# Performance work log

Measured on AMD Instinct MI355X. Metric: run time of the kernel, lower is better.

## Reference

```python
import jax, jax.numpy as jnp
import numpy as np

H = 256
OUT = 2
FANOUT = 10
RES_N = [200000, 50000, 12000, 4096]
USER_N = [250000, 60000, 20000, 8192]
B = RES_N[-1]


def setup_inputs() -> dict:
    key = jax.random.key(0)
    ks = jax.random.split(key, 40)
    ki = iter(ks)
    rng = np.random.default_rng(0)
    inp = {}
    inp["res_x"] = jax.random.normal(next(ki), (RES_N[0], H), jnp.float32)
    inp["user_x"] = jax.random.normal(next(ki), (USER_N[0], H), jnp.float32)
    for name, N in (("res", RES_N), ("user", USER_N)):
        for i in range(3):
            n_src, n_dst = N[i], N[i + 1]
            E = n_dst * FANOUT
            row = jax.random.randint(next(ki), (E,), 0, n_src)   # source node ids
            col = jnp.repeat(jnp.arange(n_dst), FANOUT)          # target node ids
            inp[f"{name}_ei{i}"] = jnp.stack([row, col]).astype(jnp.int32)
    counts = rng.integers(10, 31, size=B)                        # ragged users per restaurant
    T = int(counts.sum())
    inp["num_users_per_res"] = jnp.asarray(counts, jnp.int32)
    inp["inverse_idx"] = jax.random.randint(next(ki), (T,), 0, USER_N[-1])

    def lin(k, fi, fo):
        return jax.random.normal(k, (fo, fi), jnp.float32) / np.sqrt(fi)

    for name in ("res", "user"):
        for i in range(3):
            inp[f"{name}_Wl{i}"] = lin(next(ki), H, H)
            inp[f"{name}_bl{i}"] = jnp.zeros((H,), jnp.float32)
            inp[f"{name}_Wr{i}"] = lin(next(ki), H, H)
    inp["W_out"] = lin(next(ki), 2 * H, OUT)
    inp["b_out"] = jnp.zeros((OUT,), jnp.float32)
    return inp


def sage_conv(x_src, x_tgt, edge_index, Wl, bl, Wr):
    """PyG SAGEConv (aggr='mean', bipartite): lin_l(mean_j x_j) + lin_r(x_tgt)."""
    n_tgt = x_tgt.shape[0]
    msgs = x_src[edge_index[0]]                                            # [E, H] gather
    s = jax.ops.segment_sum(msgs, edge_index[1], num_segments=n_tgt)      # [n_tgt, H]
    cnt = jax.ops.segment_sum(jnp.ones((edge_index.shape[1],), x_src.dtype),
                              edge_index[1], num_segments=n_tgt)
    agg = s / jnp.maximum(cnt, 1.0)[:, None]
    return agg @ Wl.T + bl + x_tgt @ Wr.T


def gnn_forward(x, eis, params, N):
    # ReLU (and dropout, identity in eval) applied when i != num_layers-1 == 1
    for i, (ei, (Wl, bl, Wr)) in enumerate(zip(eis, params)):
        x_tgt = x[: N[i + 1]]
        x = sage_conv(x, x_tgt, ei, Wl, bl, Wr)
        if i != 1:
            x = jax.nn.relu(x)
    return x


def reference(res_x, user_x,
              res_ei0, res_ei1, res_ei2,
              user_ei0, user_ei1, user_ei2,
              inverse_idx, num_users_per_res,
              res_Wl0, res_bl0, res_Wr0,
              res_Wl1, res_bl1, res_Wr1,
              res_Wl2, res_bl2, res_Wr2,
              user_Wl0, user_bl0, user_Wr0,
              user_Wl1, user_bl1, user_Wr1,
              user_Wl2, user_bl2, user_Wr2,
              W_out, b_out):
    res_params = [(res_Wl0, res_bl0, res_Wr0), (res_Wl1, res_bl1, res_Wr1), (res_Wl2, res_bl2, res_Wr2)]
    user_params = [(user_Wl0, user_bl0, user_Wr0), (user_Wl1, user_bl1, user_Wr1), (user_Wl2, user_bl2, user_Wr2)]
    res_out = gnn_forward(res_x, (res_ei0, res_ei1, res_ei2), res_params, RES_N)      # [B, H]
    user_out = gnn_forward(user_x, (user_ei0, user_ei1, user_ei2), user_params, USER_N)  # [M, H]
    # ragged segment-mean pooling: split by num_users_per_res, mean each group
    u = user_out[inverse_idx]                                              # [T, H]
    T = inverse_idx.shape[0]
    seg_ids = jnp.repeat(jnp.arange(B), num_users_per_res, total_repeat_length=T)
    pooled = jax.ops.segment_sum(u, seg_ids, num_segments=B)
    pooled = pooled / num_users_per_res.astype(pooled.dtype)[:, None]      # [B, H]
    emb = jnp.concatenate([res_out, pooled], axis=1)                       # [B, 2H]
    return emb @ W_out.T + b_out
```

## Files before the change

kernel.cpp:

```cpp
#include <hip/hip_runtime.h>

#define H 256
#define FANOUT 10

typedef __attribute__((ext_vector_type(8))) short bf16x8;
typedef __attribute__((ext_vector_type(4))) float f32x4;

__device__ __forceinline__ unsigned short f2bf(float x) {
  unsigned int u = __float_as_uint(x);
  u += 0x7FFFu + ((u >> 16) & 1u);
  return (unsigned short)(u >> 16);
}
__device__ __forceinline__ float bf2f(unsigned short h) {
  return __uint_as_float(((unsigned int)h) << 16);
}

struct PtrPack { const float* p[12]; };

__global__ __launch_bounds__(256) void wprep_kernel(PtrPack pk,
                                                    unsigned short* __restrict__ WB) {
  int g = blockIdx.x * 256 + threadIdx.x;
  int mat = g >> 16;
  int e = g & 65535;
  float x = pk.p[mat][e];
  unsigned short h = f2bf(x);
  float r = x - bf2f(h);
  WB[(size_t)mat * 131072 + e] = h;
  WB[(size_t)mat * 131072 + 65536 + e] = f2bf(r);
}

__global__ __launch_bounds__(64) void agg_f32(
    const float* __restrict__ src, const int* __restrict__ row,
    unsigned short* __restrict__ ahi, unsigned short* __restrict__ alo, int n_tgt) {
  int t = blockIdx.x;
  if (t >= n_tgt) return;
  int tid = threadIdx.x;
  const int base = t * FANOUT;
  float4 acc = {0.f, 0.f, 0.f, 0.f};
#pragma unroll
  for (int k = 0; k < FANOUT; ++k) {
    int r = row[base + k];
    const float4 v = *reinterpret_cast<const float4*>(src + (size_t)r * H + tid * 4);
    acc.x += v.x; acc.y += v.y; acc.z += v.z; acc.w += v.w;
  }
  acc.x *= 0.1f; acc.y *= 0.1f; acc.z *= 0.1f; acc.w *= 0.1f;
  ushort4 h, l;
  h.x = f2bf(acc.x); l.x = f2bf(acc.x - bf2f(h.x));
  h.y = f2bf(acc.y); l.y = f2bf(acc.y - bf2f(h.y));
  h.z = f2bf(acc.z); l.z = f2bf(acc.z - bf2f(h.z));
  h.w = f2bf(acc.w); l.w = f2bf(acc.w - bf2f(h.w));
  *reinterpret_cast<ushort4*>(ahi + (size_t)t * H + tid * 4) = h;
  *reinterpret_cast<ushort4*>(alo + (size_t)t * H + tid * 4) = l;
}

__global__ __launch_bounds__(64) void agg_bf(
    const unsigned short* __restrict__ shi, const unsigned short* __restrict__ slo,
    const int* __restrict__ row,
    unsigned short* __restrict__ ahi, unsigned short* __restrict__ alo, int n_tgt) {
  int t = blockIdx.x;
  if (t >= n_tgt) return;
  int tid = threadIdx.x;
  const int base = t * FANOUT;
  float4 acc = {0.f, 0.f, 0.f, 0.f};
#pragma unroll
  for (int k = 0; k < FANOUT; ++k) {
    int r = row[base + k];
    size_t p = (size_t)r * H + tid * 4;
    const ushort4 vh = *reinterpret_cast<const ushort4*>(shi + p);
    const ushort4 vl = *reinterpret_cast<const ushort4*>(slo + p);
    acc.x += bf2f(vh.x) + bf2f(vl.x);
    acc.y += bf2f(vh.y) + bf2f(vl.y);
    acc.z += bf2f(vh.z) + bf2f(vl.z);
    acc.w += bf2f(vh.w) + bf2f(vl.w);
  }
  acc.x *= 0.1f; acc.y *= 0.1f; acc.z *= 0.1f; acc.w *= 0.1f;
  ushort4 h, l;
  h.x = f2bf(acc.x); l.x = f2bf(acc.x - bf2f(h.x));
  h.y = f2bf(acc.y); l.y = f2bf(acc.y - bf2f(h.y));
  h.z = f2bf(acc.z); l.z = f2bf(acc.z - bf2f(h.z));
  h.w = f2bf(acc.w); l.w = f2bf(acc.w - bf2f(h.w));
  *reinterpret_cast<ushort4*>(ahi + (size_t)t * H + tid * 4) = h;
  *reinterpret_cast<ushort4*>(alo + (size_t)t * H + tid * 4) = l;
}

template <int XT32>
__global__ __launch_bounds__(512, 1) void sage_gemm_mfma(
    const unsigned short* __restrict__ Ahi, const unsigned short* __restrict__ Alo,
    const unsigned short* __restrict__ Xhi, const unsigned short* __restrict__ Xlo,
    const float* __restrict__ Xf,
    const unsigned short* __restrict__ Wl2, const unsigned short* __restrict__ Wr2,
    const float* __restrict__ bias,
    unsigned short* __restrict__ Ohi, unsigned short* __restrict__ Olo,
    int n_tgt, int relu) {
  __shared__ unsigned short lds[2][2][128 * 32];
  const int tid = threadIdx.x;
  const int lane = tid & 63, wid = tid >> 6;
  const int wr = wid >> 2, wc = wid & 3;
  const int l15 = lane & 15, lk = lane >> 4;
  const int m0 = blockIdx.x * 128;
  const int srow = tid >> 2, sch = tid & 3;
  const int grow = m0 + srow;
  const bool sok = grow < n_tgt;

  f32x4 acc[4][4];
#pragma unroll
  for (int i = 0; i < 4; ++i)
#pragma unroll
    for (int j = 0; j < 4; ++j) acc[i][j] = (f32x4){0.f, 0.f, 0.f, 0.f};

  auto stage = [&](int buf, int s) {
    const int pass = s >> 3;
    const int kt = (s & 7) * 32;
    const int goff = grow * H + kt + sch * 8;
    bf16x8 vh = {0, 0, 0, 0, 0, 0, 0, 0};
    bf16x8 vl = {0, 0, 0, 0, 0, 0, 0, 0};
    if (sok) {
      if (pass == 0) {
        vh = *reinterpret_cast<const bf16x8*>(Ahi + goff);
        vl = *reinterpret_cast<const bf16x8*>(Alo + goff);
      } else if (XT32) {
        const float4 f0 = *reinterpret_cast<const float4*>(Xf + goff);
        const float4 f1 = *reinterpret_cast<const float4*>(Xf + goff + 4);
        const float xs[8] = {f0.x, f0.y, f0.z, f0.w, f1.x, f1.y, f1.z, f1.w};
#pragma unroll
        for (int i = 0; i < 8; ++i) {
          unsigned short h = f2bf(xs[i]);
          vh[i] = (short)h;
          vl[i] = (short)f2bf(xs[i] - bf2f(h));
        }
      } else {
        vh = *reinterpret_cast<const bf16x8*>(Xhi + goff);
        vl = *reinterpret_cast<const bf16x8*>(Xlo + goff);
      }
    }
    *reinterpret_cast<bf16x8*>(&lds[buf][0][srow * 32 + sch * 8]) = vh;
    *reinterpret_cast<bf16x8*>(&lds[buf][1][srow * 32 + sch * 8]) = vl;
  };

  stage(0, 0);
  __syncthreads();

  for (int s = 0; s < 16; ++s) {
    const int buf = s & 1;
    if (s < 15) stage(buf ^ 1, s + 1);
    const int pass = s >> 3;
    const int kt = (s & 7) * 32;
    const unsigned short* __restrict__ W = pass ? Wr2 : Wl2;
    bf16x8 bh[4], bl[4];
#pragma unroll
    for (int nf = 0; nf < 4; ++nf) {
      const int n = wc * 64 + nf * 16 + l15;
      const int off = n * H + kt + lk * 8;
      bh[nf] = *reinterpret_cast<const bf16x8*>(W + off);
      bl[nf] = *reinterpret_cast<const bf16x8*>(W + 65536 + off);
    }
    bf16x8 ah[4], al[4];
#pragma unroll
    for (int mf = 0; mf < 4; ++mf) {
      const int soff = (wr * 64 + mf * 16 + l15) * 32 + lk * 8;
      ah[mf] = *reinterpret_cast<const bf16x8*>(&lds[buf][0][soff]);
      al[mf] = *reinterpret_cast<const bf16x8*>(&lds[buf][1][soff]);
    }
#pragma unroll
    for (int mf = 0; mf < 4; ++mf)
#pragma unroll
      for (int nf = 0; nf < 4; ++nf) {
        acc[mf][nf] = __builtin_amdgcn_mfma_f32_16x16x32_bf16(ah[mf], bh[nf], acc[mf][nf], 0, 0, 0);
        acc[mf][nf] = __builtin_amdgcn_mfma_f32_16x16x32_bf16(ah[mf], bl[nf], acc[mf][nf], 0, 0, 0);
        acc[mf][nf] = __builtin_amdgcn_mfma_f32_16x16x32_bf16(al[mf], bh[nf], acc[mf][nf], 0, 0, 0);
      }
    __syncthreads();
  }

#pragma unroll
  for (int nf = 0; nf < 4; ++nf) {
    const int c = wc * 64 + nf * 16 + l15;
    const float bv = bias[c];
#pragma unroll
    for (int mf = 0; mf < 4; ++mf) {
      const int r0 = m0 + wr * 64 + mf * 16 + lk * 4;
#pragma unroll
      for (int j = 0; j < 4; ++j) {
        const int r = r0 + j;
        if (r < n_tgt) {
          float v = acc[mf][nf][j] + bv;
          if (relu) v = fmaxf(v, 0.f);
          unsigned short h = f2bf(v);
          Ohi[(size_t)r * H + c] = h;
          Olo[(size_t)r * H + c] = f2bf(v - bf2f(h));
        }
      }
    }
  }
}

__global__ __launch_bounds__(1024) void scan_kernel(
    const int* __restrict__ cnt, int* __restrict__ off, int B) {
  __shared__ int sdata[1024];
  const int t = threadIdx.x;
  const int base = t * 4;
  int c[4];
#pragma unroll
  for (int k = 0; k < 4; ++k) c[k] = (base + k < B) ? cnt[base + k] : 0;
  int s0 = c[0];
  int s1 = s0 + c[1];
  int s2 = s1 + c[2];
  int s3 = s2 + c[3];
  sdata[t] = s3;
  __syncthreads();
  for (int o = 1; o < 1024; o <<= 1) {
    int v = (t >= o) ? sdata[t - o] : 0;
    __syncthreads();
    sdata[t] += v;
    __syncthreads();
  }
  int excl = sdata[t] - s3;
  if (base + 0 < B) off[base + 0] = excl;
  if (base + 1 < B) off[base + 1] = excl + s0;
  if (base + 2 < B) off[base + 2] = excl + s1;
  if (base + 3 < B) off[base + 3] = excl + s2;
  if (t == 1023) off[B] = sdata[1023];
}

__global__ __launch_bounds__(64) void pool_kernel(
    const unsigned short* __restrict__ uhi, const unsigned short* __restrict__ ulo,
    const int* __restrict__ idx, const int* __restrict__ off,
    const int* __restrict__ cnt, float* __restrict__ pooled) {
  const int b = blockIdx.x;
  const int tid = threadIdx.x;
  const int o = off[b];
  const int n = cnt[b];
  float4 acc = {0.f, 0.f, 0.f, 0.f};
  for (int k = 0; k < n; ++k) {
    int u = idx[o + k];
    size_t p = (size_t)u * H + tid * 4;
    const ushort4 vh = *reinterpret_cast<const ushort4*>(uhi + p);
    const ushort4 vl = *reinterpret_cast<const ushort4*>(ulo + p);
    acc.x += bf2f(vh.x) + bf2f(vl.x);
    acc.y += bf2f(vh.y) + bf2f(vl.y);
    acc.z += bf2f(vh.z) + bf2f(vl.z);
    acc.w += bf2f(vh.w) + bf2f(vl.w);
  }
  const float inv = 1.0f / (float)n;
  acc.x *= inv; acc.y *= inv; acc.z *= inv; acc.w *= inv;
  *reinterpret_cast<float4*>(pooled + (size_t)b * H + tid * 4) = acc;
}

__global__ __launch_bounds__(256) void out_kernel(
    const unsigned short* __restrict__ rhi, const unsigned short* __restrict__ rlo,
    const float* __restrict__ pooled,
    const float* __restrict__ Wout, const float* __restrict__ bout,
    float* __restrict__ out) {
  const int b = blockIdx.x;
  const int t = threadIdx.x;
  const float e0 = bf2f(rhi[(size_t)b * H + t]) + bf2f(rlo[(size_t)b * H + t]);
  const float e1 = pooled[(size_t)b * H + t];
  float p0 = e0 * Wout[t] + e1 * Wout[256 + t];
  float p1 = e0 * Wout[512 + t] + e1 * Wout[768 + t];
#pragma unroll
  for (int o = 32; o >= 1; o >>= 1) {
    p0 += __shfl_down(p0, o, 64);
    p1 += __shfl_down(p1, o, 64);
  }
  __shared__ float s0[4], s1[4];
  const int w = t >> 6, lane = t & 63;
  if (lane == 0) { s0[w] = p0; s1[w] = p1; }
  __syncthreads();
  if (t == 0) out[(size_t)b * 2 + 0] = s0[0] + s0[1] + s0[2] + s0[3] + bout[0];
  if (t == 1) out[(size_t)b * 2 + 1] = s1[0] + s1[1] + s1[2] + s1[3] + bout[1];
}

extern "C" void kernel_launch(void* const* d_in, const int* in_sizes, int n_in,
                              void* d_out, int out_size, void* d_ws,
                              size_t ws_size, hipStream_t stream) {
  const float* res_x  = (const float*)d_in[0];
  const float* user_x = (const float*)d_in[1];
  const int* res_ei[3]  = {(const int*)d_in[2], (const int*)d_in[3], (const int*)d_in[4]};
  const int* user_ei[3] = {(const int*)d_in[5], (const int*)d_in[6], (const int*)d_in[7]};

  const int* counts;
  const int* inv_idx;
  if (in_sizes[8] == 4096) { counts = (const int*)d_in[8]; inv_idx = (const int*)d_in[9]; }
  else                     { counts = (const int*)d_in[9]; inv_idx = (const int*)d_in[8]; }

  const float* rW[9]; const float* uW[9];
  for (int i = 0; i < 9; ++i) rW[i] = (const float*)d_in[10 + i];
  for (int i = 0; i < 9; ++i) uW[i] = (const float*)d_in[19 + i];
  const float* Wout = (const float*)d_in[28];
  const float* bout = (const float*)d_in[29];

  unsigned short* u = (unsigned short*)d_ws;
  const size_t P0 = (size_t)60000 * H;
  const size_t P2 = (size_t)20000 * H;
  const size_t P3 = (size_t)8192 * H;
  const size_t P4 = (size_t)4096 * H;
  unsigned short* AGGh = u;
  unsigned short* AGGl = u + P0;
  unsigned short* B1h  = u + 2 * P0;
  unsigned short* B1l  = u + 3 * P0;
  unsigned short* B2h  = u + 4 * P0;
  unsigned short* B2l  = u + 4 * P0 + P2;
  unsigned short* U3h  = u + 4 * P0 + 2 * P2;
  unsigned short* U3l  = u + 4 * P0 + 2 * P2 + P3;
  unsigned short* R3h  = u + 4 * P0 + 2 * P2 + 2 * P3;
  unsigned short* R3l  = u + 4 * P0 + 2 * P2 + 2 * P3 + P4;
  unsigned short* WB   = u + 4 * P0 + 2 * P2 + 2 * P3 + 2 * P4;
  int* OFF             = (int*)(WB + (size_t)12 * 131072);
  float* POOL          = (float*)B2h;

  PtrPack pk;
  pk.p[0] = uW[0]; pk.p[1] = uW[2];
  pk.p[2] = uW[3]; pk.p[3] = uW[5];
  pk.p[4] = uW[6]; pk.p[5] = uW[8];
  pk.p[6] = rW[0]; pk.p[7] = rW[2];
  pk.p[8] = rW[3]; pk.p[9] = rW[5];
  pk.p[10] = rW[6]; pk.p[11] = rW[8];
  wprep_kernel<<<3072, 256, 0, stream>>>(pk, WB);

  auto Wm = [&](int m) { return WB + (size_t)m * 131072; };
  auto grid = [](int n) { return (n + 127) / 128; };

  agg_f32<<<60000, 64, 0, stream>>>(user_x, user_ei[0], AGGh, AGGl, 60000);
  sage_gemm_mfma<1><<<grid(60000), 512, 0, stream>>>(
      AGGh, AGGl, nullptr, nullptr, user_x, Wm(0), Wm(1), uW[1], B1h, B1l, 60000, 1);
  agg_bf<<<20000, 64, 0, stream>>>(B1h, B1l, user_ei[1], AGGh, AGGl, 20000);
  sage_gemm_mfma<0><<<grid(20000), 512, 0, stream>>>(
      AGGh, AGGl, B1h, B1l, nullptr, Wm(2), Wm(3), uW[4], B2h, B2l, 20000, 0);
  agg_bf<<<8192, 64, 0, stream>>>(B2h, B2l, user_ei[2], AGGh, AGGl, 8192);
  sage_gemm_mfma<0><<<grid(8192), 512, 0, stream>>>(
      AGGh, AGGl, B2h, B2l, nullptr, Wm(4), Wm(5), uW[7], U3h, U3l, 8192, 1);

  agg_f32<<<50000, 64, 0, stream>>>(res_x, res_ei[0], AGGh, AGGl, 50000);
  sage_gemm_mfma<1><<<grid(50000), 512, 0, stream>>>(
      AGGh, AGGl, nullptr, nullptr, res_x, Wm(6), Wm(7), rW[1], B1h, B1l, 50000, 1);
  agg_bf<<<12000, 64, 0, stream>>>(B1h, B1l, res_ei[1], AGGh, AGGl, 12000);
  sage_gemm_mfma<0><<<grid(12000), 512, 0, stream>>>(
      AGGh, AGGl, B1h, B1l, nullptr, Wm(8), Wm(9), rW[4], B2h, B2l, 12000, 0);
  agg_bf<<<4096, 64, 0, stream>>>(B2h, B2l, res_ei[2], AGGh, AGGl, 4096);
  sage_gemm_mfma<0><<<grid(4096), 512, 0, stream>>>(
      AGGh, AGGl, B2h, B2l, nullptr, Wm(10), Wm(11), rW[7], R3h, R3l, 4096, 1);

  scan_kernel<<<1, 1024, 0, stream>>>(counts, OFF, 4096);
  pool_kernel<<<4096, 64, 0, stream>>>(U3h, U3l, inv_idx, OFF, counts, POOL);
  out_kernel<<<4096, 256, 0, stream>>>(R3h, R3l, POOL, Wout, bout, (float*)d_out);
}
```

Before: 1.164 ms.

## Store intermediates as fp32, convert to bf16 split inside GEMM staging

Result: faster. 1.068 ms (-8.3%).

```diff
diff --git a/kernel.cpp b/kernel.cpp
--- a/kernel.cpp
+++ b/kernel.cpp
@@ -29,78 +29,39 @@
   WB[(size_t)mat * 131072 + 65536 + e] = f2bf(r);
 }
 
-__global__ __launch_bounds__(64) void agg_f32(
+__global__ __launch_bounds__(256) void agg_kernel(
     const float* __restrict__ src, const int* __restrict__ row,
-    unsigned short* __restrict__ ahi, unsigned short* __restrict__ alo, int n_tgt) {
-  int t = blockIdx.x;
+    float* __restrict__ agg, int n_tgt) {
+  const int t = blockIdx.x * 4 + (threadIdx.x >> 6);
   if (t >= n_tgt) return;
-  int tid = threadIdx.x;
+  const int lane = threadIdx.x & 63;
   const int base = t * FANOUT;
   float4 acc = {0.f, 0.f, 0.f, 0.f};
 #pragma unroll
   for (int k = 0; k < FANOUT; ++k) {
     int r = row[base + k];
-    const float4 v = *reinterpret_cast<const float4*>(src + (size_t)r * H + tid * 4);
+    const float4 v =
+        *reinterpret_cast<const float4*>(src + (size_t)r * H + lane * 4);
     acc.x += v.x; acc.y += v.y; acc.z += v.z; acc.w += v.w;
   }
   acc.x *= 0.1f; acc.y *= 0.1f; acc.z *= 0.1f; acc.w *= 0.1f;
-  ushort4 h, l;
-  h.x = f2bf(acc.x); l.x = f2bf(acc.x - bf2f(h.x));
-  h.y = f2bf(acc.y); l.y = f2bf(acc.y - bf2f(h.y));
-  h.z = f2bf(acc.z); l.z = f2bf(acc.z - bf2f(h.z));
-  h.w = f2bf(acc.w); l.w = f2bf(acc.w - bf2f(h.w));
-  *reinterpret_cast<ushort4*>(ahi + (size_t)t * H + tid * 4) = h;
-  *reinterpret_cast<ushort4*>(alo + (size_t)t * H + tid * 4) = l;
-}
-
-__global__ __launch_bounds__(64) void agg_bf(
-    const unsigned short* __restrict__ shi, const unsigned short* __restrict__ slo,
-    const int* __restrict__ row,
-    unsigned short* __restrict__ ahi, unsigned short* __restrict__ alo, int n_tgt) {
-  int t = blockIdx.x;
-  if (t >= n_tgt) return;
-  int tid = threadIdx.x;
-  const int base = t * FANOUT;
-  float4 acc = {0.f, 0.f, 0.f, 0.f};
-#pragma unroll
-  for (int k = 0; k < FANOUT; ++k) {
-    int r = row[base + k];
-    size_t p = (size_t)r * H + tid * 4;
-    const ushort4 vh = *reinterpret_cast<const ushort4*>(shi + p);
-    const ushort4 vl = *reinterpret_cast<const ushort4*>(slo + p);
-    acc.x += bf2f(vh.x) + bf2f(vl.x);
-    acc.y += bf2f(vh.y) + bf2f(vl.y);
-    acc.z += bf2f(vh.z) + bf2f(vl.z);
-    acc.w += bf2f(vh.w) + bf2f(vl.w);
-  }
-  acc.x *= 0.1f; acc.y *= 0.1f; acc.z *= 0.1f; acc.w *= 0.1f;
-  ushort4 h, l;
-  h.x = f2bf(acc.x); l.x = f2bf(acc.x - bf2f(h.x));
-  h.y = f2bf(acc.y); l.y = f2bf(acc.y - bf2f(h.y));
-  h.z = f2bf(acc.z); l.z = f2bf(acc.z - bf2f(h.z));
-  h.w = f2bf(acc.w); l.w = f2bf(acc.w - bf2f(h.w));
-  *reinterpret_cast<ushort4*>(ahi + (size_t)t * H + tid * 4) = h;
-  *reinterpret_cast<ushort4*>(alo + (size_t)t * H + tid * 4) = l;
-}
-
-template <int XT32>
-__global__ __launch_bounds__(512, 1) void sage_gemm_mfma(
-    const unsigned short* __restrict__ Ahi, const unsigned short* __restrict__ Alo,
-    const unsigned short* __restrict__ Xhi, const unsigned short* __restrict__ Xlo,
-    const float* __restrict__ Xf,
+  *reinterpret_cast<float4*>(agg + (size_t)t * H + lane * 4) = acc;
+}
+
+__global__ __launch_bounds__(256, 2) void sage_gemm_mfma(
+    const float* __restrict__ Af, const float* __restrict__ Xf,
     const unsigned short* __restrict__ Wl2, const unsigned short* __restrict__ Wr2,
-    const float* __restrict__ bias,
-    unsigned short* __restrict__ Ohi, unsigned short* __restrict__ Olo,
+    const float* __restrict__ bias, float* __restrict__ Out,
     int n_tgt, int relu) {
-  __shared__ unsigned short lds[2][2][128 * 32];
+  __shared__ unsigned short lds[2][2][4 * 64 * 8];
   const int tid = threadIdx.x;
-  const int lane = tid & 63, wid = tid >> 6;
-  const int wr = wid >> 2, wc = wid & 3;
+  const int lane = tid & 63, wc = tid >> 6;
   const int l15 = lane & 15, lk = lane >> 4;
-  const int m0 = blockIdx.x * 128;
+  const int m0 = blockIdx.x * 64;
   const int srow = tid >> 2, sch = tid & 3;
   const int grow = m0 + srow;
   const bool sok = grow < n_tgt;
+  const int ldsoff = (((srow >> 4) * 64) + (srow & 15) + sch * 16) * 8;
 
   f32x4 acc[4][4];
 #pragma unroll
@@ -108,58 +69,53 @@
 #pragma unroll
     for (int j = 0; j < 4; ++j) acc[i][j] = (f32x4){0.f, 0.f, 0.f, 0.f};
 
-  auto stage = [&](int buf, int s) {
-    const int pass = s >> 3;
-    const int kt = (s & 7) * 32;
-    const int goff = grow * H + kt + sch * 8;
-    bf16x8 vh = {0, 0, 0, 0, 0, 0, 0, 0};
-    bf16x8 vl = {0, 0, 0, 0, 0, 0, 0, 0};
+  float4 f0 = {0, 0, 0, 0}, f1 = {0, 0, 0, 0};
+  auto gload = [&](int s) {
     if (sok) {
-      if (pass == 0) {
-        vh = *reinterpret_cast<const bf16x8*>(Ahi + goff);
-        vl = *reinterpret_cast<const bf16x8*>(Alo + goff);
-      } else if (XT32) {
-        const float4 f0 = *reinterpret_cast<const float4*>(Xf + goff);
-        const float4 f1 = *reinterpret_cast<const float4*>(Xf + goff + 4);
-        const float xs[8] = {f0.x, f0.y, f0.z, f0.w, f1.x, f1.y, f1.z, f1.w};
-#pragma unroll
-        for (int i = 0; i < 8; ++i) {
-          unsigned short h = f2bf(xs[i]);
-          vh[i] = (short)h;
-          vl[i] = (short)f2bf(xs[i] - bf2f(h));
-        }
-      } else {
-        vh = *reinterpret_cast<const bf16x8*>(Xhi + goff);
-        vl = *reinterpret_cast<const bf16x8*>(Xlo + goff);
-      }
-    }
-    *reinterpret_cast<bf16x8*>(&lds[buf][0][srow * 32 + sch * 8]) = vh;
-    *reinterpret_cast<bf16x8*>(&lds[buf][1][srow * 32 + sch * 8]) = vl;
+      const float* S = (s >> 3) ? Xf : Af;
+      const float* p = S + (size_t)grow * H + (s & 7) * 32 + sch * 8;
+      f0 = *reinterpret_cast<const float4*>(p);
+      f1 = *reinterpret_cast<const float4*>(p + 4);
+    } else {
+      f0 = (float4){0, 0, 0, 0};
+      f1 = (float4){0, 0, 0, 0};
+    }
   };
-
-  stage(0, 0);
+  auto sconv = [&](int buf) {
+    const float xs[8] = {f0.x, f0.y, f0.z, f0.w, f1.x, f1.y, f1.z, f1.w};
+    bf16x8 vh, vl;
+#pragma unroll
+    for (int i = 0; i < 8; ++i) {
+      unsigned short h = f2bf(xs[i]);
+      vh[i] = (short)h;
+      vl[i] = (short)f2bf(xs[i] - bf2f(h));
+    }
+    *reinterpret_cast<bf16x8*>(&lds[buf][0][ldsoff]) = vh;
+    *reinterpret_cast<bf16x8*>(&lds[buf][1][ldsoff]) = vl;
+  };
+
+  gload(0);
+  sconv(0);
   __syncthreads();
 
   for (int s = 0; s < 16; ++s) {
     const int buf = s & 1;
-    if (s < 15) stage(buf ^ 1, s + 1);
-    const int pass = s >> 3;
+    if (s < 15) gload(s + 1);
     const int kt = (s & 7) * 32;
-    const unsigned short* __restrict__ W = pass ? Wr2 : Wl2;
+    const unsigned short* __restrict__ W = (s >> 3) ? Wr2 : Wl2;
     bf16x8 bh[4], bl[4];
 #pragma unroll
     for (int nf = 0; nf < 4; ++nf) {
-      const int n = wc * 64 + nf * 16 + l15;
-      const int off = n * H + kt + lk * 8;
+      const int off = (wc * 64 + nf * 16 + l15) * H + kt + lk * 8;
       bh[nf] = *reinterpret_cast<const bf16x8*>(W + off);
       bl[nf] = *reinterpret_cast<const bf16x8*>(W + 65536 + off);
     }
     bf16x8 ah[4], al[4];
 #pragma unroll
     for (int mf = 0; mf < 4; ++mf) {
-      const int soff = (wr * 64 + mf * 16 + l15) * 32 + lk * 8;
-      ah[mf] = *reinterpret_cast<const bf16x8*>(&lds[buf][0][soff]);
-      al[mf] = *reinterpret_cast<const bf16x8*>(&lds[buf][1][soff]);
+      const int o = (mf * 64 + lane) * 8;
+      ah[mf] = *reinterpret_cast<const bf16x8*>(&lds[buf][0][o]);
+      al[mf] = *reinterpret_cast<const bf16x8*>(&lds[buf][1][o]);
     }
 #pragma unroll
     for (int mf = 0; mf < 4; ++mf)
@@ -169,6 +125,7 @@
         acc[mf][nf] = __builtin_amdgcn_mfma_f32_16x16x32_bf16(ah[mf], bl[nf], acc[mf][nf], 0, 0, 0);
         acc[mf][nf] = __builtin_amdgcn_mfma_f32_16x16x32_bf16(al[mf], bh[nf], acc[mf][nf], 0, 0, 0);
       }
+    if (s < 15) sconv(buf ^ 1);
     __syncthreads();
   }
 
@@ -178,16 +135,14 @@
     const float bv = bias[c];
 #pragma unroll
     for (int mf = 0; mf < 4; ++mf) {
-      const int r0 = m0 + wr * 64 + mf * 16 + lk * 4;
+      const int r0 = m0 + mf * 16 + lk * 4;
 #pragma unroll
       for (int j = 0; j < 4; ++j) {
         const int r = r0 + j;
         if (r < n_tgt) {
           float v = acc[mf][nf][j] + bv;
           if (relu) v = fmaxf(v, 0.f);
-          unsigned short h = f2bf(v);
-          Ohi[(size_t)r * H + c] = h;
-          Olo[(size_t)r * H + c] = f2bf(v - bf2f(h));
+          Out[(size_t)r * H + c] = v;
         }
       }
     }
@@ -222,38 +177,33 @@
   if (t == 1023) off[B] = sdata[1023];
 }
 
-__global__ __launch_bounds__(64) void pool_kernel(
-    const unsigned short* __restrict__ uhi, const unsigned short* __restrict__ ulo,
-    const int* __restrict__ idx, const int* __restrict__ off,
-    const int* __restrict__ cnt, float* __restrict__ pooled) {
-  const int b = blockIdx.x;
-  const int tid = threadIdx.x;
+__global__ __launch_bounds__(256) void pool_kernel(
+    const float* __restrict__ uo, const int* __restrict__ idx,
+    const int* __restrict__ off, const int* __restrict__ cnt,
+    float* __restrict__ pooled) {
+  const int b = blockIdx.x * 4 + (threadIdx.x >> 6);
+  const int lane = threadIdx.x & 63;
   const int o = off[b];
   const int n = cnt[b];
   float4 acc = {0.f, 0.f, 0.f, 0.f};
   for (int k = 0; k < n; ++k) {
     int u = idx[o + k];
-    size_t p = (size_t)u * H + tid * 4;
-    const ushort4 vh = *reinterpret_cast<const ushort4*>(uhi + p);
-    const ushort4 vl = *reinterpret_cast<const ushort4*>(ulo + p);
-    acc.x += bf2f(vh.x) + bf2f(vl.x);
-    acc.y += bf2f(vh.y) + bf2f(vl.y);
-    acc.z += bf2f(vh.z) + bf2f(vl.z);
-    acc.w += bf2f(vh.w) + bf2f(vl.w);
+    const float4 v =
+        *reinterpret_cast<const float4*>(uo + (size_t)u * H + lane * 4);
+    acc.x += v.x; acc.y += v.y; acc.z += v.z; acc.w += v.w;
   }
   const float inv = 1.0f / (float)n;
   acc.x *= inv; acc.y *= inv; acc.z *= inv; acc.w *= inv;
-  *reinterpret_cast<float4*>(pooled + (size_t)b * H + tid * 4) = acc;
+  *reinterpret_cast<float4*>(pooled + (size_t)b * H + lane * 4) = acc;
 }
 
 __global__ __launch_bounds__(256) void out_kernel(
-    const unsigned short* __restrict__ rhi, const unsigned short* __restrict__ rlo,
-    const float* __restrict__ pooled,
+    const float* __restrict__ res_out, const float* __restrict__ pooled,
     const float* __restrict__ Wout, const float* __restrict__ bout,
     float* __restrict__ out) {
   const int b = blockIdx.x;
   const int t = threadIdx.x;
-  const float e0 = bf2f(rhi[(size_t)b * H + t]) + bf2f(rlo[(size_t)b * H + t]);
+  const float e0 = res_out[(size_t)b * H + t];
   const float e1 = pooled[(size_t)b * H + t];
   float p0 = e0 * Wout[t] + e1 * Wout[256 + t];
   float p1 = e0 * Wout[512 + t] + e1 * Wout[768 + t];
@@ -289,24 +239,15 @@
   const float* Wout = (const float*)d_in[28];
   const float* bout = (const float*)d_in[29];
 
-  unsigned short* u = (unsigned short*)d_ws;
-  const size_t P0 = (size_t)60000 * H;
-  const size_t P2 = (size_t)20000 * H;
-  const size_t P3 = (size_t)8192 * H;
-  const size_t P4 = (size_t)4096 * H;
-  unsigned short* AGGh = u;
-  unsigned short* AGGl = u + P0;
-  unsigned short* B1h  = u + 2 * P0;
-  unsigned short* B1l  = u + 3 * P0;
-  unsigned short* B2h  = u + 4 * P0;
-  unsigned short* B2l  = u + 4 * P0 + P2;
-  unsigned short* U3h  = u + 4 * P0 + 2 * P2;
-  unsigned short* U3l  = u + 4 * P0 + 2 * P2 + P3;
-  unsigned short* R3h  = u + 4 * P0 + 2 * P2 + 2 * P3;
-  unsigned short* R3l  = u + 4 * P0 + 2 * P2 + 2 * P3 + P4;
-  unsigned short* WB   = u + 4 * P0 + 2 * P2 + 2 * P3 + 2 * P4;
-  int* OFF             = (int*)(WB + (size_t)12 * 131072);
-  float* POOL          = (float*)B2h;
+  float* ws = (float*)d_ws;
+  float* AGG  = ws;
+  float* B1   = AGG  + (size_t)60000 * H;
+  float* B2   = B1   + (size_t)60000 * H;
+  float* U3   = B2   + (size_t)20000 * H;
+  float* R3   = U3   + (size_t)8192  * H;
+  float* POOL = R3   + (size_t)4096  * H;
+  unsigned short* WB = (unsigned short*)(POOL + (size_t)4096 * H);
+  int* OFF = (int*)(WB + (size_t)12 * 131072);
 
   PtrPack pk;
   pk.p[0] = uW[0]; pk.p[1] = uW[2];
@@ -318,29 +259,30 @@
   wprep_kernel<<<3072, 256, 0, stream>>>(pk, WB);
 
   auto Wm = [&](int m) { return WB + (size_t)m * 131072; };
-  auto grid = [](int n) { return (n + 127) / 128; };
-
-  agg_f32<<<60000, 64, 0, stream>>>(user_x, user_ei[0], AGGh, AGGl, 60000);
-  sage_gemm_mfma<1><<<grid(60000), 512, 0, stream>>>(
-      AGGh, AGGl, nullptr, nullptr, user_x, Wm(0), Wm(1), uW[1], B1h, B1l, 60000, 1);
-  agg_bf<<<20000, 64, 0, stream>>>(B1h, B1l, user_ei[1], AGGh, AGGl, 20000);
-  sage_gemm_mfma<0><<<grid(20000), 512, 0, stream>>>(
-      AGGh, AGGl, B1h, B1l, nullptr, Wm(2), Wm(3), uW[4], B2h, B2l, 20000, 0);
-  agg_bf<<<8192, 64, 0, stream>>>(B2h, B2l, user_ei[2], AGGh, AGGl, 8192);
-  sage_gemm_mfma<0><<<grid(8192), 512, 0, stream>>>(
-      AGGh, AGGl, B2h, B2l, nullptr, Wm(4), Wm(5), uW[7], U3h, U3l, 8192, 1);
-
-  agg_f32<<<50000, 64, 0, stream>>>(res_x, res_ei[0], AGGh, AGGl, 50000);
-  sage_gemm_mfma<1><<<grid(50000), 512, 0, stream>>>(
-      AGGh, AGGl, nullptr, nullptr, res_x, Wm(6), Wm(7), rW[1], B1h, B1l, 50000, 1);
-  agg_bf<<<12000, 64, 0, stream>>>(B1h, B1l, res_ei[1], AGGh, AGGl, 12000);
-  sage_gemm_mfma<0><<<grid(12000), 512, 0, stream>>>(
-      AGGh, AGGl, B1h, B1l, nullptr, Wm(8), Wm(9), rW[4], B2h, B2l, 12000, 0);
-  agg_bf<<<4096, 64, 0, stream>>>(B2h, B2l, res_ei[2], AGGh, AGGl, 4096);
-  sage_gemm_mfma<0><<<grid(4096), 512, 0, stream>>>(
-      AGGh, AGGl, B2h, B2l, nullptr, Wm(10), Wm(11), rW[7], R3h, R3l, 4096, 1);
+  auto gemm_grid = [](int n) { return (n + 63) / 64; };
+  auto agg_grid = [](int n) { return (n + 3) / 4; };
+
+  agg_kernel<<<agg_grid(60000), 256, 0, stream>>>(user_x, user_ei[0], AGG, 60000);
+  sage_gemm_mfma<<<gemm_grid(60000), 256, 0, stream>>>(
+      AGG, user_x, Wm(0), Wm(1), uW[1], B1, 60000, 1);
+  agg_kernel<<<agg_grid(20000), 256, 0, stream>>>(B1, user_ei[1], AGG, 20000);
+  sage_gemm_mfma<<<gemm_grid(20000), 256, 0, stream>>>(
+      AGG, B1, Wm(2), Wm(3), uW[4], B2, 20000, 0);
+  agg_kernel<<<agg_grid(8192), 256, 0, stream>>>(B2, user_ei[2], AGG, 8192);
+  sage_gemm_mfma<<<gemm_grid(8192), 256, 0, stream>>>(
+      AGG, B2, Wm(4), Wm(5), uW[7], U3, 8192, 1);
+
+  agg_kernel<<<agg_grid(50000), 256, 0, stream>>>(res_x, res_ei[0], AGG, 50000);
+  sage_gemm_mfma<<<gemm_grid(50000), 256, 0, stream>>>(
+      AGG, res_x, Wm(6), Wm(7), rW[1], B1, 50000, 1);
+  agg_kernel<<<agg_grid(12000), 256, 0, stream>>>(B1, res_ei[1], AGG, 12000);
+  sage_gemm_mfma<<<gemm_grid(12000), 256, 0, stream>>>(
+      AGG, B1, Wm(8), Wm(9), rW[4], B2, 12000, 0);
+  agg_kernel<<<agg_grid(4096), 256, 0, stream>>>(B2, res_ei[2], AGG, 4096);
+  sage_gemm_mfma<<<gemm_grid(4096), 256, 0, stream>>>(
+      AGG, B2, Wm(10), Wm(11), rW[7], R3, 4096, 1);
 
   scan_kernel<<<1, 1024, 0, stream>>>(counts, OFF, 4096);
-  pool_kernel<<<4096, 64, 0, stream>>>(U3h, U3l, inv_idx, OFF, counts, POOL);
-  out_kernel<<<4096, 256, 0, stream>>>(R3h, R3l, POOL, Wout, bout, (float*)d_out);
-}
+  pool_kernel<<<1024, 256, 0, stream>>>(U3, inv_idx, OFF, counts, POOL);
+  out_kernel<<<4096, 256, 0, stream>>>(R3, POOL, Wout, bout, (float*)d_out);
+}
```
